# Kernel tuning notes

Hardware: AMD Instinct MI355X
Metric: run time of the kernel (lower is better)

## Reference

```python
import jax, jax.numpy as jnp
import numpy as np

B, S, E = 2, 2048, 2048
H, G = 16, 4
HD = E // H  # 128 head dim


def setup_inputs() -> dict:
    key = jax.random.key(0)
    k1, k2, k3, k4 = jax.random.split(key, 4)
    x = jax.random.normal(k1, (B, S, E), dtype=jnp.float32)
    mask = jnp.zeros((B, 1, S, S), dtype=jnp.float32)
    # torch nn.Linear weights stored as [in, out] for x @ W
    W1 = jax.random.normal(k2, (E, 2 * G * HD), dtype=jnp.float32) * 0.02
    W2 = jax.random.normal(k3, (E, E), dtype=jnp.float32) * 0.02
    W3 = jax.random.normal(k4, (E, E), dtype=jnp.float32) * 0.02
    return {"x": x, "mask": mask, "W1": W1, "W2": W2, "W3": W3}


def reference(x, mask, W1, W2, W3):
    b, s, e_model = x.shape
    hd = e_model // H
    # linear_1 -> rearrange 'b s (n g e) -> n b g s e'
    kv = (x @ W1).reshape(b, s, 2, G, hd).transpose(2, 0, 3, 1, 4)
    k, v = kv[0], kv[1]  # [b, g, s, e]
    # linear_2 -> 'b t (h e) -> b h t e'
    q = (x @ W2).reshape(b, s, H, hd).transpose(0, 2, 1, 3)  # [b, h, t, e]
    # NOTE: g is summed out here, exactly as in the source einsum (no sqrt scaling)
    score = jnp.einsum('bhte,bgse->bhts', q, k)
    score = jax.nn.softmax(score + mask, axis=-1)
    out = jnp.einsum('bhts,bgse->bthe', score, v)  # g summed again
    out = out.reshape(b, s, e_model)
    return out @ W3
```

## Files before the change

### kernel.cpp

```cpp
#include <hip/hip_runtime.h>
#include <cstdint>

#define S_LEN 2048
#define EMB   2048
#define NHEAD 16
#define HDIM  128
#define NFUSE 2304
#define LOG2E 1.4426950408889634f

typedef __attribute__((ext_vector_type(8))) _Float16 h8;
typedef __attribute__((ext_vector_type(4))) _Float16 h4;
typedef __attribute__((ext_vector_type(8))) short short8;
typedef __attribute__((ext_vector_type(4))) short short4v;
typedef __attribute__((ext_vector_type(4))) float f32x4;
typedef unsigned int u32;

__device__ inline short f2bf(float x) {
  union { float f; uint32_t u; } v; v.f = x;
  uint32_t r = v.u + 0x7fffu + ((v.u >> 16) & 1u);
  return (short)(r >> 16);
}
__device__ inline float bf2f(short b) {
  union { uint32_t u; float f; } v; v.u = ((uint32_t)(uint16_t)b) << 16;
  return v.f;
}
__device__ inline float fexp2(float x) {
  float r;
  __asm__ volatile("v_exp_f32 %0, %1" : "=v"(r) : "v"(x));
  return r;
}
__device__ inline u32 pkrtz(float a, float b) {
  u32 r;
  __asm__ volatile("v_cvt_pkrtz_f16_f32 %0, %1, %2" : "=v"(r) : "v"(a), "v"(b));
  return r;
}
__device__ inline void glds16(const void* g, void* l) {
  __builtin_amdgcn_global_load_lds(
      (const __attribute__((address_space(1))) u32*)g,
      (__attribute__((address_space(3))) u32*)l, 16, 0, 0);
}

__global__ __launch_bounds__(256) void cvt_xm_kernel(
    const float* __restrict__ x, _Float16* __restrict__ xf,
    const float* __restrict__ mask, short* __restrict__ maskb) {
  int bid = blockIdx.x;
  if (bid < 8192) {
    size_t idx = (size_t)bid * 256 + threadIdx.x;
    float4 v = *(const float4*)(x + idx * 4);
    h4 o;
    o[0] = (_Float16)v.x; o[1] = (_Float16)v.y;
    o[2] = (_Float16)v.z; o[3] = (_Float16)v.w;
    *(h4*)(xf + idx * 4) = o;
  } else {
    size_t idx = (size_t)(bid - 8192) * 256 + threadIdx.x;
    float4 v = *(const float4*)(mask + idx * 4);
    short4v o;
    o[0] = f2bf(v.x * LOG2E); o[1] = f2bf(v.y * LOG2E);
    o[2] = f2bf(v.z * LOG2E); o[3] = f2bf(v.w * LOG2E);
    *(short4v*)(maskb + idx * 4) = o;
  }
}

__global__ __launch_bounds__(256) void transpose_f16_kernel(
    const float* __restrict__ W, _Float16* __restrict__ T, int K, int N) {
  __shared__ float Tt[64][65];
  const int tid = threadIdx.x;
  const int k0 = blockIdx.y * 64, n0 = blockIdx.x * 64;
  {
    int r = tid >> 2, c0 = (tid & 3) * 16;
    const float* src = W + (size_t)(k0 + r) * N + n0 + c0;
#pragma unroll
    for (int j = 0; j < 4; ++j) {
      float4 v = *(const float4*)(src + 4 * j);
      Tt[r][c0 + 4 * j + 0] = v.x; Tt[r][c0 + 4 * j + 1] = v.y;
      Tt[r][c0 + 4 * j + 2] = v.z; Tt[r][c0 + 4 * j + 3] = v.w;
    }
  }
  __syncthreads();
  {
    int n = tid >> 2, kc = (tid & 3) * 16;
    h8 o0, o1;
#pragma unroll
    for (int i = 0; i < 8; ++i) {
      o0[i] = (_Float16)Tt[kc + i][n];
      o1[i] = (_Float16)Tt[kc + 8 + i][n];
    }
    size_t off = (size_t)(n0 + n) * K + k0 + kc;
    *(h8*)(T + off) = o0;
    *(h8*)(T + off + 8) = o1;
  }
}

__global__ __launch_bounds__(256) void transpose_wkv_kernel(
    const float* __restrict__ W1, _Float16* __restrict__ T) {
  __shared__ float Tt[64][65];
  const int tid = threadIdx.x;
  const int k0 = blockIdx.y * 64, n0 = blockIdx.x * 64;
  {
    int r = tid >> 2, c0 = (tid & 3) * 16;
    int base = n0 + c0 + ((n0 >= 128) ? 384 : 0);
    const float* src = W1 + (size_t)(k0 + r) * 1024 + base;
#pragma unroll
    for (int j = 0; j < 4; ++j) {
      float4 s0 = *(const float4*)(src + 4 * j);
      float4 s1 = *(const float4*)(src + 128 + 4 * j);
      float4 s2 = *(const float4*)(src + 256 + 4 * j);
      float4 s3 = *(const float4*)(src + 384 + 4 * j);
      Tt[r][c0 + 4 * j + 0] = (s0.x + s1.x) + (s2.x + s3.x);
      Tt[r][c0 + 4 * j + 1] = (s0.y + s1.y) + (s2.y + s3.y);
      Tt[r][c0 + 4 * j + 2] = (s0.z + s1.z) + (s2.z + s3.z);
      Tt[r][c0 + 4 * j + 3] = (s0.w + s1.w) + (s2.w + s3.w);
    }
  }
  __syncthreads();
  {
    int n = tid >> 2, kc = (tid & 3) * 16;
    h8 o0, o1;
#pragma unroll
    for (int i = 0; i < 8; ++i) {
      o0[i] = (_Float16)Tt[kc + i][n];
      o1[i] = (_Float16)Tt[kc + 8 + i][n];
    }
    size_t off = (size_t)(n0 + n) * 2048 + k0 + kc;
    *(h8*)(T + off) = o0;
    *(h8*)(T + off + 8) = o1;
  }
}

template <bool QSCALE>
__global__ __launch_bounds__(256, 3) void gemm_f16(
    const _Float16* __restrict__ A, const _Float16* __restrict__ Bt,
    float* __restrict__ C, _Float16* __restrict__ Cf,
    int M, int N, int K, int qlim) {
  extern __shared__ char smraw[];
  _Float16* sm = (_Float16*)smraw;
  const int BUFS = 8192;

  const int tid  = threadIdx.x;
  const int w    = tid >> 6;
  const int lane = tid & 63;
  const int quad = lane >> 4, col16 = lane & 15;

  const int nwgx = gridDim.x;
  const int id   = blockIdx.y * nwgx + blockIdx.x;
  const int cpx  = (nwgx * gridDim.y) >> 3;
  const int sid  = (id & 7) * cpx + (id >> 3);
  const int bx   = sid % nwgx, by = sid / nwgx;

  const int row0 = by * 128, col0 = bx * 128;
  const float esc = (col0 < qlim) ? LOG2E : 1.0f;

  const int srow  = w * 32 + (lane >> 2);
  const int kpart = (lane & 3) * 8;
  const _Float16* pA0 = A + (size_t)(row0 + srow) * K + kpart;
  const _Float16* pA1 = pA0 + (size_t)16 * K;
  const _Float16* pB0 = Bt + (size_t)(col0 + srow) * K + kpart;
  const _Float16* pB1 = pB0 + (size_t)16 * K;

  const int oA0 = (w * 32) * 32, oA1 = (w * 32 + 16) * 32;
  const int oB0 = 4096 + (w * 32) * 32, oB1 = 4096 + (w * 32 + 16) * 32;

#define STAGE_GEMM(bo)                                                        \
  do {                                                                        \
    glds16(pA0, sm + (bo) + oA0); glds16(pA1, sm + (bo) + oA1);               \
    glds16(pB0, sm + (bo) + oB0); glds16(pB1, sm + (bo) + oB1);               \
    pA0 += 32; pA1 += 32; pB0 += 32; pB1 += 32;                               \
  } while (0)

  f32x4 acc[2][8];
#pragma unroll
  for (int mt = 0; mt < 2; ++mt)
#pragma unroll
    for (int nt = 0; nt < 8; ++nt) {
      acc[mt][nt][0] = 0.f; acc[mt][nt][1] = 0.f;
      acc[mt][nt][2] = 0.f; acc[mt][nt][3] = 0.f;
    }

  const int nchunk = K >> 5;
  int bo = 0;
  STAGE_GEMM(0);

#pragma unroll 1
  for (int c = 0; c < nchunk; ++c) {
    if (c + 1 < nchunk) {
      STAGE_GEMM(bo ^ BUFS);
      __asm__ volatile("s_waitcnt vmcnt(4)" ::: "memory");
    } else {
      __asm__ volatile("s_waitcnt vmcnt(0)" ::: "memory");
    }
    __builtin_amdgcn_s_barrier();

    const _Float16* AS = sm + bo;
    const _Float16* BS = sm + bo + 4096;

    h8 af[2];
#pragma unroll
    for (int mt = 0; mt < 2; ++mt)
      af[mt] = *(const h8*)&AS[(w * 32 + mt * 16 + col16) * 32 + quad * 8];
#pragma unroll
    for (int nt = 0; nt < 8; ++nt) {
      h8 b8 = *(const h8*)&BS[(nt * 16 + col16) * 32 + quad * 8];
#pragma unroll
      for (int mt = 0; mt < 2; ++mt)
        acc[mt][nt] = __builtin_amdgcn_mfma_f32_16x16x32_f16(af[mt], b8, acc[mt][nt], 0, 0, 0);
    }
    __builtin_amdgcn_s_barrier();
    bo ^= BUFS;
  }
#undef STAGE_GEMM

#pragma unroll
  for (int mt = 0; mt < 2; ++mt)
#pragma unroll
    for (int nt = 0; nt < 8; ++nt)
#pragma unroll
      for (int r = 0; r < 4; ++r) {
        int row = row0 + w * 32 + mt * 16 + quad * 4 + r;
        int col = col0 + nt * 16 + col16;
        float v = acc[mt][nt][r];
        if constexpr (QSCALE) {
          Cf[(size_t)row * N + col] = (_Float16)(v * esc);
        } else {
          C[(size_t)row * N + col] = v;
        }
      }
}

__global__ __launch_bounds__(256) void build_vt(
    const short* __restrict__ QKh, short* __restrict__ VT) {
  __shared__ short T[64][136];
  const int tid = threadIdx.x;
  const int gs = blockIdx.x * 64;
  const int b = gs >> 11;
  const int s = gs & 2047;
  {
    int r = tid >> 2, c0 = (tid & 3) * 32;
    const short* src = QKh + (size_t)(gs + r) * NFUSE + 2176 + c0;
#pragma unroll
    for (int j = 0; j < 4; ++j)
      *(short8*)&T[r][c0 + 8 * j] = *(const short8*)(src + 8 * j);
  }
  __syncthreads();
  {
    int d = tid >> 1, c = (tid & 1) * 32;
    short* dst = VT + (size_t)(b * HDIM + d) * S_LEN + s + c;
#pragma unroll
    for (int jo = 0; jo < 4; ++jo) {
      short8 o;
#pragma unroll
      for (int i = 0; i < 8; ++i) o[i] = T[c + jo * 8 + i][d];
      *(short8*)(dst + jo * 8) = o;
    }
  }
}

__global__ __launch_bounds__(256, 2) void flash_f16(
    const _Float16* __restrict__ QKf, const _Float16* __restrict__ VT,
    const short* __restrict__ maskb, _Float16* __restrict__ AO) {
  __shared__ _Float16 KS[64 * 128];
  __shared__ _Float16 VtS[128 * 64];
  __shared__ _Float16 PsS[2 * 4 * 16 * 64];
  __shared__ short    MkS[4 * 32 * 64];

  const int tid   = threadIdx.x;
  const int w     = tid >> 6;
  const int lane  = tid & 63;
  const int quad  = lane >> 4;
  const int col16 = lane & 15;
  const int xq    = col16 & 7;
  const int bh = blockIdx.y, b = bh >> 4, h = bh & 15;
  const int t0 = blockIdx.x * 128;

  const int jr = lane >> 4;
  const int kg = lane & 15;
  const int vr = lane >> 3;
  const int vg = lane & 7;

  _Float16* myK = KS + w * 2048;
  _Float16* myV = VtS + w * 2048;
  short*    myM = MkS + w * 2048;

  h8 qf[2][4];
#pragma unroll
  for (int t = 0; t < 2; ++t) {
#pragma unroll
    for (int j = 0; j < 4; ++j) {
      int rl = 4 * j + jr;
      int gq = kg ^ (rl & 7);
      size_t go = (size_t)(b * S_LEN + t0 + 64 * t + 16 * w + rl) * NFUSE
                + h * HDIM + gq * 8;
      glds16(QKf + go, myK + j * 512);
    }
    __asm__ volatile("s_waitcnt vmcnt(0)" ::: "memory");
#pragma unroll
    for (int c = 0; c < 4; ++c)
      qf[t][c] = *(const h8*)&myK[col16 * 128 + (((c * 4 + quad) ^ xq) * 8)];
    __asm__ volatile("s_waitcnt lgkmcnt(0)" ::: "memory");
  }

  const _Float16* Kbase = QKf + (size_t)b * S_LEN * NFUSE + 2048;
  const _Float16* Vbase = VT + (size_t)b * HDIM * S_LEN;
  const short*    Mbase = maskb + (size_t)b * S_LEN * S_LEN;
  u32 offK[4], offV[4], offM[4];
#pragma unroll
  for (int j = 0; j < 4; ++j) {
    int rl = 4 * j + jr;
    offK[j] = (u32)(16 * w + rl) * NFUSE + (u32)((kg ^ (rl & 7)) * 8);
    int dl = 32 * w + 8 * j + vr;
    offV[j] = (u32)dl * S_LEN + (u32)((vg ^ (vr & 7)) * 8);
    int mrw = j * 8 + (lane >> 3);
    int mq  = t0 + 64 * (mrw >> 4) + 16 * w + (mrw & 15);
    offM[j] = (u32)mq * S_LEN + (u32)(((lane & 7) ^ (mrw & 7)) * 8);
  }

#pragma unroll
  for (int j = 0; j < 4; ++j) glds16(Kbase + offK[j], myK + j * 512);
#pragma unroll
  for (int j = 0; j < 4; ++j) glds16(Mbase + offM[j], myM + j * 512);
#pragma unroll
  for (int j = 0; j < 4; ++j) glds16(Vbase + offV[j], myV + j * 512);
#pragma unroll
  for (int j = 0; j < 4; ++j) {
    offK[j] += 64 * NFUSE; offM[j] += 64; offV[j] += 64;
  }

  f32x4 oacc[2][8];
#pragma unroll
  for (int t = 0; t < 2; ++t)
#pragma unroll
    for (int d = 0; d < 8; ++d) {
      oacc[t][d][0] = 0.f; oacc[t][d][1] = 0.f;
      oacc[t][d][2] = 0.f; oacc[t][d][3] = 0.f;
    }
  float mrow[2] = {-3.0e38f, -3.0e38f};
  float lrow[2] = {0.f, 0.f};

#pragma unroll 1
  for (int it = 0; it < S_LEN / 64; ++it) {
    __asm__ volatile("s_waitcnt vmcnt(8)" ::: "memory");
    __builtin_amdgcn_s_barrier();

    f32x4 sacc[2][4];
#pragma unroll
    for (int t = 0; t < 2; ++t)
#pragma unroll
      for (int nt = 0; nt < 4; ++nt) {
        sacc[t][nt][0] = 0.f; sacc[t][nt][1] = 0.f;
        sacc[t][nt][2] = 0.f; sacc[t][nt][3] = 0.f;
      }
    __builtin_amdgcn_s_setprio(1);
#pragma unroll
    for (int c = 0; c < 4; ++c)
#pragma unroll
      for (int nt = 0; nt < 4; ++nt) {
        h8 k8 = *(const h8*)&KS[(nt * 16 + col16) * 128 + (((c * 4 + quad) ^ xq) * 8)];
#pragma unroll
        for (int t = 0; t < 2; ++t)
          sacc[t][nt] = __builtin_amdgcn_mfma_f32_16x16x32_f16(k8, qf[t][c], sacc[t][nt], 0, 0, 0);
      }
    __builtin_amdgcn_s_setprio(0);

    __asm__ volatile("s_waitcnt vmcnt(0)" ::: "memory");
    short4v msk[2][4];
#pragma unroll
    for (int t = 0; t < 2; ++t)
#pragma unroll
      for (int nt = 0; nt < 4; ++nt)
        msk[t][nt] = *(const short4v*)
            &myM[(t * 16 + col16) * 64 + (((quad + nt * 4) ^ (xq << 1)) << 2)];
    __asm__ volatile("s_waitcnt lgkmcnt(0)" ::: "memory");
    __builtin_amdgcn_s_barrier();

    if (it + 1 < S_LEN / 64) {
#pragma unroll
      for (int j = 0; j < 4; ++j) glds16(Kbase + offK[j], myK + j * 512);
#pragma unroll
      for (int j = 0; j < 4; ++j) glds16(Mbase + offM[j], myM + j * 512);
#pragma unroll
      for (int j = 0; j < 4; ++j) { offK[j] += 64 * NFUSE; offM[j] += 64; }
    }

#pragma unroll
    for (int t = 0; t < 2; ++t) {
      float vv[4][4];
#pragma unroll
      for (int nt = 0; nt < 4; ++nt)
#pragma unroll
        for (int r = 0; r < 4; ++r)
          vv[nt][r] = sacc[t][nt][r] + bf2f(msk[t][nt][r]);
      float mx = vv[0][0];
#pragma unroll
      for (int nt = 0; nt < 4; ++nt)
#pragma unroll
        for (int r = 0; r < 4; ++r) mx = fmaxf(mx, vv[nt][r]);
      mx = fmaxf(mx, __shfl_xor(mx, 16));
      mx = fmaxf(mx, __shfl_xor(mx, 32));

      float nm = fmaxf(mrow[t], mx);
      if (__all(mx - mrow[t] <= 8.0f)) {
        nm = mrow[t];
      } else {
        float al = fexp2(mrow[t] - nm);
        lrow[t] *= al;
#pragma unroll
        for (int d = 0; d < 8; ++d) {
          oacc[t][d][0] *= al; oacc[t][d][1] *= al;
          oacc[t][d][2] *= al; oacc[t][d][3] *= al;
        }
        mrow[t] = nm;
      }

      float ps = 0.f;
      u32 pk0[4], pk1[4];
#pragma unroll
      for (int nt = 0; nt < 4; ++nt) {
        float p0 = fexp2(vv[nt][0] - nm);
        float p1 = fexp2(vv[nt][1] - nm);
        float p2 = fexp2(vv[nt][2] - nm);
        float p3 = fexp2(vv[nt][3] - nm);
        ps += (p0 + p1) + (p2 + p3);
        pk0[nt] = pkrtz(p0, p1);
        pk1[nt] = pkrtz(p2, p3);
      }
      ps += __shfl_xor(ps, 16);
      ps += __shfl_xor(ps, 32);
      lrow[t] += ps;

      int pbase = ((t * 4 + w) * 16 + col16) * 64 + (quad & 1) * 4;
#pragma unroll
      for (int nt = 0; nt < 4; ++nt) {
        uint2 pv2; pv2.x = pk0[nt]; pv2.y = pk1[nt];
        *(uint2*)&PsS[pbase + (((2 * nt + (quad >> 1)) ^ xq) * 8)] = pv2;
      }
    }

    __asm__ volatile("s_waitcnt lgkmcnt(0)" ::: "memory");
    h8 pa[2][2];
#pragma unroll
    for (int t = 0; t < 2; ++t) {
      int pb = ((t * 4 + w) * 16 + col16) * 64;
      pa[t][0] = *(const h8*)&PsS[pb + ((quad ^ xq) * 8)];
      pa[t][1] = *(const h8*)&PsS[pb + (((4 + quad) ^ xq) * 8)];
    }
    __builtin_amdgcn_s_setprio(1);
#pragma unroll
    for (int d = 0; d < 8; ++d) {
      int vo = (d * 16 + col16) * 64;
      h8 vb0 = *(const h8*)&VtS[vo + ((quad ^ xq) * 8)];
      h8 vb1 = *(const h8*)&VtS[vo + (((4 + quad) ^ xq) * 8)];
#pragma unroll
      for (int t = 0; t < 2; ++t) {
        oacc[t][d] = __builtin_amdgcn_mfma_f32_16x16x32_f16(vb0, pa[t][0], oacc[t][d], 0, 0, 0);
        oacc[t][d] = __builtin_amdgcn_mfma_f32_16x16x32_f16(vb1, pa[t][1], oacc[t][d], 0, 0, 0);
      }
    }
    __builtin_amdgcn_s_setprio(0);

    __builtin_amdgcn_s_barrier();
    if (it + 1 < S_LEN / 64) {
#pragma unroll
      for (int j = 0; j < 4; ++j) glds16(Vbase + offV[j], myV + j * 512);
#pragma unroll
      for (int j = 0; j < 4; ++j) offV[j] += 64;
    }
  }

#pragma unroll
  for (int t = 0; t < 2; ++t) {
    float inv = 1.0f / lrow[t];
    int q = t0 + 64 * t + 16 * w + col16;
    _Float16* dst = AO + (size_t)(b * S_LEN + q) * EMB + h * HDIM + quad * 4;
#pragma unroll
    for (int d = 0; d < 8; ++d) {
      h4 o4;
#pragma unroll
      for (int r = 0; r < 4; ++r) o4[r] = (_Float16)(oacc[t][d][r] * inv);
      *(h4*)(dst + d * 16) = o4;
    }
  }
}

extern "C" void kernel_launch(void* const* d_in, const int* in_sizes, int n_in,
                              void* d_out, int out_size, void* d_ws, size_t ws_size,
                              hipStream_t stream) {
  const float* x    = (const float*)d_in[0];
  const float* mask = (const float*)d_in[1];
  const float* W1   = (const float*)d_in[2];
  const float* W2   = (const float*)d_in[3];
  const float* W3   = (const float*)d_in[4];
  float* out = (float*)d_out;

  char* ws = (char*)d_ws;
  size_t off = 0;
  _Float16* xf   = (_Float16*)(ws + off); off += (size_t)4096 * 2048 * 2;
  _Float16* Wtf  = (_Float16*)(ws + off); off += (size_t)NFUSE * 2048 * 2;
  _Float16* QKf  = (_Float16*)(ws + off); off += (size_t)4096 * NFUSE * 2;
  _Float16* VT   = (_Float16*)(ws + off); off += (size_t)2 * 128 * 2048 * 2;
  _Float16* AOf  = (_Float16*)(ws + off); off += (size_t)4096 * 2048 * 2;
  short*    maskb= (short*)(ws + off);    off += (size_t)2 * 2048 * 2048 * 2;
  _Float16* W3t  = xf;

  cvt_xm_kernel<<<16384, 256, 0, stream>>>(x, xf, mask, maskb);
  transpose_f16_kernel<<<dim3(32, 32), 256, 0, stream>>>(W2, Wtf, 2048, 2048);
  transpose_wkv_kernel<<<dim3(4, 32), 256, 0, stream>>>(
      W1, Wtf + (size_t)2048 * 2048);

  gemm_f16<true><<<dim3(NFUSE / 128, 32), 256, 32768, stream>>>(
      xf, Wtf, nullptr, QKf, 4096, NFUSE, 2048, 2048);

  build_vt<<<64, 256, 0, stream>>>((const short*)QKf, (short*)VT);

  flash_f16<<<dim3(S_LEN / 128, 2 * NHEAD), 256, 0, stream>>>(
      QKf, VT, maskb, AOf);

  transpose_f16_kernel<<<dim3(32, 32), 256, 0, stream>>>(W3, W3t, 2048, 2048);
  gemm_f16<false><<<dim3(16, 32), 256, 32768, stream>>>(
      AOf, W3t, out, nullptr, 4096, 2048, 2048, 0);
}
```

Baseline: 346.5 us.

## Merge weight transposes into one launch and fuse V transpose into GEMM epilogue

Combines the W2, W3 and W1 transpose kernels into a single launch, giving W3t its own workspace buffer instead of aliasing xf. Removes the separate build_vt kernel by having the QKV GEMM tile covering the V columns write its accumulator transposed via shared memory directly into VT. This cuts kernel launches and an extra global read/write of V, at the cost of slightly more dynamic shared memory per GEMM block and extra workspace.

```diff
diff --git a/kernel.cpp b/kernel.cpp
--- a/kernel.cpp
+++ b/kernel.cpp
@@ -61,42 +61,33 @@
   }
 }
 
-__global__ __launch_bounds__(256) void transpose_f16_kernel(
-    const float* __restrict__ W, _Float16* __restrict__ T, int K, int N) {
+__global__ __launch_bounds__(256) void transpose_all_kernel(
+    const float* __restrict__ W2, const float* __restrict__ W3,
+    const float* __restrict__ W1, _Float16* __restrict__ Wtf,
+    _Float16* __restrict__ W3t) {
   __shared__ float Tt[64][65];
   const int tid = threadIdx.x;
-  const int k0 = blockIdx.y * 64, n0 = blockIdx.x * 64;
-  {
+  const int blk = blockIdx.x;
+
+  _Float16* T;
+  int k0, n0;
+  if (blk < 2048) {
+    const float* W = (blk < 1024) ? W2 : W3;
+    int b = blk & 1023;
+    n0 = (b & 31) * 64; k0 = (b >> 5) * 64;
+    T = (blk < 1024) ? Wtf : W3t;
     int r = tid >> 2, c0 = (tid & 3) * 16;
-    const float* src = W + (size_t)(k0 + r) * N + n0 + c0;
+    const float* src = W + (size_t)(k0 + r) * 2048 + n0 + c0;
 #pragma unroll
     for (int j = 0; j < 4; ++j) {
       float4 v = *(const float4*)(src + 4 * j);
       Tt[r][c0 + 4 * j + 0] = v.x; Tt[r][c0 + 4 * j + 1] = v.y;
       Tt[r][c0 + 4 * j + 2] = v.z; Tt[r][c0 + 4 * j + 3] = v.w;
     }
-  }
-  __syncthreads();
-  {
-    int n = tid >> 2, kc = (tid & 3) * 16;
-    h8 o0, o1;
-#pragma unroll
-    for (int i = 0; i < 8; ++i) {
-      o0[i] = (_Float16)Tt[kc + i][n];
-      o1[i] = (_Float16)Tt[kc + 8 + i][n];
-    }
-    size_t off = (size_t)(n0 + n) * K + k0 + kc;
-    *(h8*)(T + off) = o0;
-    *(h8*)(T + off + 8) = o1;
-  }
-}
-
-__global__ __launch_bounds__(256) void transpose_wkv_kernel(
-    const float* __restrict__ W1, _Float16* __restrict__ T) {
-  __shared__ float Tt[64][65];
-  const int tid = threadIdx.x;
-  const int k0 = blockIdx.y * 64, n0 = blockIdx.x * 64;
-  {
+  } else {
+    int b = blk - 2048;
+    n0 = (b & 3) * 64; k0 = (b >> 2) * 64;
+    T = Wtf + (size_t)2048 * 2048;
     int r = tid >> 2, c0 = (tid & 3) * 16;
     int base = n0 + c0 + ((n0 >= 128) ? 384 : 0);
     const float* src = W1 + (size_t)(k0 + r) * 1024 + base;
@@ -131,7 +122,7 @@
 __global__ __launch_bounds__(256, 3) void gemm_f16(
     const _Float16* __restrict__ A, const _Float16* __restrict__ Bt,
     float* __restrict__ C, _Float16* __restrict__ Cf,
-    int M, int N, int K, int qlim) {
+    _Float16* __restrict__ VTp, int M, int N, int K, int qlim) {
   extern __shared__ char smraw[];
   _Float16* sm = (_Float16*)smraw;
   const int BUFS = 8192;
@@ -208,6 +199,30 @@
     bo ^= BUFS;
   }
 #undef STAGE_GEMM
+
+  if constexpr (QSCALE) {
+    if (col0 == 2176) {
+      __syncthreads();
+      _Float16* smt = sm;
+#pragma unroll
+      for (int mt = 0; mt < 2; ++mt)
+#pragma unroll
+        for (int nt = 0; nt < 8; ++nt)
+#pragma unroll
+          for (int r = 0; r < 4; ++r)
+            smt[(nt * 16 + col16) * 136 + (w * 32 + mt * 16 + quad * 4 + r)] =
+                (_Float16)acc[mt][nt][r];
+      __syncthreads();
+      int d = tid >> 1, half = tid & 1;
+      const _Float16* src = smt + d * 136 + half * 64;
+      _Float16* dst = VTp + ((size_t)(row0 >> 11) * HDIM + d) * S_LEN
+                    + (row0 & 2047) + half * 64;
+#pragma unroll
+      for (int j = 0; j < 8; ++j)
+        *(h8*)(dst + j * 8) = *(const h8*)(src + j * 8);
+      return;
+    }
+  }
 
 #pragma unroll
   for (int mt = 0; mt < 2; ++mt)
@@ -226,34 +241,6 @@
       }
 }
 
-__global__ __launch_bounds__(256) void build_vt(
-    const short* __restrict__ QKh, short* __restrict__ VT) {
-  __shared__ short T[64][136];
-  const int tid = threadIdx.x;
-  const int gs = blockIdx.x * 64;
-  const int b = gs >> 11;
-  const int s = gs & 2047;
-  {
-    int r = tid >> 2, c0 = (tid & 3) * 32;
-    const short* src = QKh + (size_t)(gs + r) * NFUSE + 2176 + c0;
-#pragma unroll
-    for (int j = 0; j < 4; ++j)
-      *(short8*)&T[r][c0 + 8 * j] = *(const short8*)(src + 8 * j);
-  }
-  __syncthreads();
-  {
-    int d = tid >> 1, c = (tid & 1) * 32;
-    short* dst = VT + (size_t)(b * HDIM + d) * S_LEN + s + c;
-#pragma unroll
-    for (int jo = 0; jo < 4; ++jo) {
-      short8 o;
-#pragma unroll
-      for (int i = 0; i < 8; ++i) o[i] = T[c + jo * 8 + i][d];
-      *(short8*)(dst + jo * 8) = o;
-    }
-  }
-}
-
 __global__ __launch_bounds__(256, 2) void flash_f16(
     const _Float16* __restrict__ QKf, const _Float16* __restrict__ VT,
     const short* __restrict__ maskb, _Float16* __restrict__ AO) {
@@ -498,22 +485,17 @@
   _Float16* VT   = (_Float16*)(ws + off); off += (size_t)2 * 128 * 2048 * 2;
   _Float16* AOf  = (_Float16*)(ws + off); off += (size_t)4096 * 2048 * 2;
   short*    maskb= (short*)(ws + off);    off += (size_t)2 * 2048 * 2048 * 2;
-  _Float16* W3t  = xf;
+  _Float16* W3t  = (_Float16*)(ws + off); off += (size_t)2048 * 2048 * 2;
 
   cvt_xm_kernel<<<16384, 256, 0, stream>>>(x, xf, mask, maskb);
-  transpose_f16_kernel<<<dim3(32, 32), 256, 0, stream>>>(W2, Wtf, 2048, 2048);
-  transpose_wkv_kernel<<<dim3(4, 32), 256, 0, stream>>>(
-      W1, Wtf + (size_t)2048 * 2048);
-
-  gemm_f16<true><<<dim3(NFUSE / 128, 32), 256, 32768, stream>>>(
-      xf, Wtf, nullptr, QKf, 4096, NFUSE, 2048, 2048);
-
-  build_vt<<<64, 256, 0, stream>>>((const short*)QKf, (short*)VT);
+  transpose_all_kernel<<<2176, 256, 0, stream>>>(W2, W3, W1, Wtf, W3t);
+
+  gemm_f16<true><<<dim3(NFUSE / 128, 32), 256, 35840, stream>>>(
+      xf, Wtf, nullptr, QKf, VT, 4096, NFUSE, 2048, 2048);
 
   flash_f16<<<dim3(S_LEN / 128, 2 * NHEAD), 256, 0, stream>>>(
       QKf, VT, maskb, AOf);
 
-  transpose_f16_kernel<<<dim3(32, 32), 256, 0, stream>>>(W3, W3t, 2048, 2048);
   gemm_f16<false><<<dim3(16, 32), 256, 32768, stream>>>(
-      AOf, W3t, out, nullptr, 4096, 2048, 2048, 0);
-}
+      AOf, W3t, out, nullptr, nullptr, 4096, 2048, 2048, 0);
+}
```

Measured after the change: 355.6 us. 2.6% more time.
